# Kernel optimization log

Measured on AMD Instinct MI355X. Metric: run time of the kernel, lower is better.

The kernel has to match this reference:

```python
import jax, jax.numpy as jnp
import numpy as np

B, C, H, W = 32, 256, 56, 56
HIDDEN = 512  # int(channels * hidden_ratio) = int(256 * 2.0)
RANK = 8


def setup_inputs() -> dict:
    key = jax.random.key(0)
    k_x, k1, k2, kA, kB = jax.random.split(key, 5)
    x = jax.random.normal(k_x, (B, C, H, W), dtype=jnp.float32)
    # nn.Linear weights are (out_features, in_features)
    w1 = jax.random.normal(k1, (HIDDEN, C), dtype=jnp.float32) * (1.0 / np.sqrt(C))
    w2 = jax.random.normal(k2, (C, HIDDEN), dtype=jnp.float32) * (1.0 / np.sqrt(HIDDEN))
    wA = jax.random.normal(kA, (H * RANK, C), dtype=jnp.float32) * (1.0 / np.sqrt(C))
    wB = jax.random.normal(kB, (RANK * W, C), dtype=jnp.float32) * (1.0 / np.sqrt(C))
    return {"x": x, "w1": w1, "w2": w2, "wA": wA, "wB": wB}


def reference(x, w1, w2, wA, wB):
    # Global average pool over spatial dims: (B, C)
    y = jnp.mean(x, axis=(2, 3))
    # MLP with exact GELU (dropout = identity at inference)
    h = jax.nn.gelu(y @ w1.T, approximate=False)        # (B, HIDDEN)
    y_prime = jax.nn.gelu(h @ w2.T, approximate=False)  # (B, C)
    # y_rep broadcasts y_prime[b] to every channel, so the per-channel
    # projections are identical across c: compute once per batch.
    A = (y_prime @ wA.T).reshape(B, H, RANK)   # (B, H, r)
    Bm = (y_prime @ wB.T).reshape(B, RANK, W)  # (B, r, W)
    M = jnp.einsum('bik,bkj->bij', A, Bm)      # (B, H, W)
    attn = jax.nn.sigmoid(M)
    # Broadcast identical map across channels -> (B, C, H, W)
    return jnp.broadcast_to(attn[:, None, :, :], (B, C, H, W))
```

## Files before the change

kernel.cpp:

```cpp
#include <hip/hip_runtime.h>
#include <math.h>

#define BB   32
#define CC   256
#define HH   56
#define WW   56
#define HID  512
#define RNK  8
#define HWN  (HH * WW)
#define HW4  (HWN / 4)

__device__ __forceinline__ float gelu_exact(float v) {
    return 0.5f * v * (1.0f + erff(v * 0.70710678118654752f));
}
__device__ __forceinline__ float dot4(float4 a, float4 b) {
    return a.x * b.x + a.y * b.y + a.z * b.z + a.w * b.w;
}

__global__ __launch_bounds__(256) void pool_kernel(const float* __restrict__ x,
                                                   float* __restrict__ y) {
    const int bc  = blockIdx.x;
    const int tid = threadIdx.x;
    const float4* xp = reinterpret_cast<const float4*>(x) + (size_t)bc * HW4;

    float s = 0.0f;
    for (int p = tid; p < HW4; p += 256) {
        float4 v = xp[p];
        s += (v.x + v.y) + (v.z + v.w);
    }
    #pragma unroll
    for (int off = 32; off > 0; off >>= 1) s += __shfl_down(s, off, 64);

    __shared__ float ls[4];
    const int wave = tid >> 6;
    if ((tid & 63) == 0) ls[wave] = s;
    __syncthreads();
    if (tid == 0) {
        float t = (ls[0] + ls[1]) + (ls[2] + ls[3]);
        y[bc] = t * (1.0f / (float)HWN);
    }
}

__global__ __launch_bounds__(1024) void middle_kernel(
        const float* __restrict__ y,  const float* __restrict__ w1,
        const float* __restrict__ w2, const float* __restrict__ wA,
        const float* __restrict__ wB, float* __restrict__ attn) {
    const int b    = blockIdx.x;
    const int tid  = threadIdx.x;
    const int wv   = tid >> 6;
    const int lane = tid & 63;
    const int sub  = lane & 15;
    const int rg   = lane >> 4;

    __shared__ float y_s[CC];
    __shared__ float h_s[HID];
    __shared__ float yp_s[CC];
    __shared__ float ab_s[896];

    if (tid < CC) y_s[tid] = y[b * CC + tid];
    __syncthreads();

    {
        const float4* ys4 = reinterpret_cast<const float4*>(y_s);
        const float4 yv0 = ys4[sub],      yv1 = ys4[sub + 16],
                     yv2 = ys4[sub + 32], yv3 = ys4[sub + 48];
        for (int row = wv * 4 + rg; row < HID; row += 64) {
            const float4* wr = reinterpret_cast<const float4*>(w1 + (size_t)row * CC);
            float d = dot4(wr[sub], yv0)      + dot4(wr[sub + 16], yv1)
                    + dot4(wr[sub + 32], yv2) + dot4(wr[sub + 48], yv3);
            #pragma unroll
            for (int m = 8; m > 0; m >>= 1) d += __shfl_xor(d, m, 64);
            if (sub == 0) h_s[row] = gelu_exact(d);
        }
    }
    __syncthreads();

    {
        const float4* hs4 = reinterpret_cast<const float4*>(h_s);
        float4 hv[8];
        #pragma unroll
        for (int k = 0; k < 8; ++k) hv[k] = hs4[sub + 16 * k];
        for (int row = wv * 4 + rg; row < CC; row += 64) {
            const float4* wr = reinterpret_cast<const float4*>(w2 + (size_t)row * HID);
            float d = 0.0f;
            #pragma unroll
            for (int k = 0; k < 8; ++k) d += dot4(wr[sub + 16 * k], hv[k]);
            #pragma unroll
            for (int m = 8; m > 0; m >>= 1) d += __shfl_xor(d, m, 64);
            if (sub == 0) yp_s[row] = gelu_exact(d);
        }
    }
    __syncthreads();

    {
        const float4* ps4 = reinterpret_cast<const float4*>(yp_s);
        const float4 pv0 = ps4[sub],      pv1 = ps4[sub + 16],
                     pv2 = ps4[sub + 32], pv3 = ps4[sub + 48];
        for (int row = wv * 4 + rg; row < 896; row += 64) {
            const float* W = (row < 448) ? (wA + (size_t)row * CC)
                                         : (wB + (size_t)(row - 448) * CC);
            const float4* wr = reinterpret_cast<const float4*>(W);
            float d = dot4(wr[sub], pv0)      + dot4(wr[sub + 16], pv1)
                    + dot4(wr[sub + 32], pv2) + dot4(wr[sub + 48], pv3);
            #pragma unroll
            for (int m = 8; m > 0; m >>= 1) d += __shfl_xor(d, m, 64);
            if (sub == 0) ab_s[row] = d;
        }
    }
    __syncthreads();

    for (int p = tid; p < HWN; p += 1024) {
        const int i = p / WW;
        const int j = p - i * WW;
        float m = 0.0f;
        #pragma unroll
        for (int r = 0; r < RNK; ++r) m += ab_s[i * RNK + r] * ab_s[448 + r * WW + j];
        attn[(size_t)b * HWN + p] = 1.0f / (1.0f + expf(-m));
    }
}

__global__ __launch_bounds__(256) void bcast_kernel(const float* __restrict__ attn,
                                                    float4* __restrict__ out) {
    const unsigned total  = (unsigned)BB * CC * HW4;
    const unsigned stride = gridDim.x * blockDim.x;
    const float4* ap = reinterpret_cast<const float4*>(attn);
    for (unsigned idx = blockIdx.x * blockDim.x + threadIdx.x; idx < total;
         idx += stride) {
        const unsigned b = idx / (CC * HW4);
        const unsigned p = idx % HW4;
        out[idx] = ap[b * HW4 + p];
    }
}

extern "C" void kernel_launch(void* const* d_in, const int* in_sizes, int n_in,
                              void* d_out, int out_size, void* d_ws, size_t ws_size,
                              hipStream_t stream) {
    const float* x  = (const float*)d_in[0];
    const float* w1 = (const float*)d_in[1];
    const float* w2 = (const float*)d_in[2];
    const float* wA = (const float*)d_in[3];
    const float* wB = (const float*)d_in[4];
    float* out = (float*)d_out;

    float* y    = (float*)d_ws;
    float* attn = y + BB * CC;

    pool_kernel<<<BB * CC, 256, 0, stream>>>(x, y);
    middle_kernel<<<BB, 1024, 0, stream>>>(y, w1, w2, wA, wB, attn);
    bcast_kernel<<<2048, 256, 0, stream>>>(attn, reinterpret_cast<float4*>(out));
}
```

Baseline: 61.72 us.

## Split middle MLP across 8 blocks per batch and fuse attention map into broadcast

The middle kernel now runs 8 blocks per batch. Each block recomputes the two MLP layers with all 1024 threads mapped to rows in fixed passes, then computes only its slice of the wA/wB projection rows. The sigmoid attention map is moved into the broadcast kernel: each block rebuilds the full map in shared memory and writes it to 32 channels, which removes the attn round trip through global memory. In exchange the MLP weights are read 8 times redundantly, and the map is recomputed 8 times per batch.

After: 52.46 us. 15.0% less time.

```diff
diff --git a/kernel.cpp b/kernel.cpp
--- a/kernel.cpp
+++ b/kernel.cpp
@@ -44,69 +44,93 @@
 __global__ __launch_bounds__(1024) void middle_kernel(
         const float* __restrict__ y,  const float* __restrict__ w1,
         const float* __restrict__ w2, const float* __restrict__ wA,
-        const float* __restrict__ wB, float* __restrict__ attn) {
-    const int b    = blockIdx.x;
-    const int tid  = threadIdx.x;
-    const int wv   = tid >> 6;
-    const int lane = tid & 63;
-    const int sub  = lane & 15;
-    const int rg   = lane >> 4;
+        const float* __restrict__ wB, float* __restrict__ ab) {
+    const int b     = blockIdx.x >> 3;
+    const int slice = blockIdx.x & 7;
+    const int tid   = threadIdx.x;
 
     __shared__ float y_s[CC];
     __shared__ float h_s[HID];
     __shared__ float yp_s[CC];
-    __shared__ float ab_s[896];
 
     if (tid < CC) y_s[tid] = y[b * CC + tid];
     __syncthreads();
 
     {
+        const int sub = tid & 7;
+        const int rg  = tid >> 3;
         const float4* ys4 = reinterpret_cast<const float4*>(y_s);
-        const float4 yv0 = ys4[sub],      yv1 = ys4[sub + 16],
-                     yv2 = ys4[sub + 32], yv3 = ys4[sub + 48];
-        for (int row = wv * 4 + rg; row < HID; row += 64) {
+        float4 yv[8];
+        #pragma unroll
+        for (int k = 0; k < 8; ++k) yv[k] = ys4[sub + 8 * k];
+        #pragma unroll
+        for (int pass = 0; pass < 4; ++pass) {
+            const int row = pass * 128 + rg;
             const float4* wr = reinterpret_cast<const float4*>(w1 + (size_t)row * CC);
-            float d = dot4(wr[sub], yv0)      + dot4(wr[sub + 16], yv1)
-                    + dot4(wr[sub + 32], yv2) + dot4(wr[sub + 48], yv3);
+            float d = 0.0f;
             #pragma unroll
-            for (int m = 8; m > 0; m >>= 1) d += __shfl_xor(d, m, 64);
+            for (int k = 0; k < 8; ++k) d += dot4(wr[sub + 8 * k], yv[k]);
+            d += __shfl_xor(d, 1, 64);
+            d += __shfl_xor(d, 2, 64);
+            d += __shfl_xor(d, 4, 64);
             if (sub == 0) h_s[row] = gelu_exact(d);
         }
     }
     __syncthreads();
 
     {
+        const int sub = tid & 15;
+        const int rg  = tid >> 4;
         const float4* hs4 = reinterpret_cast<const float4*>(h_s);
         float4 hv[8];
         #pragma unroll
         for (int k = 0; k < 8; ++k) hv[k] = hs4[sub + 16 * k];
-        for (int row = wv * 4 + rg; row < CC; row += 64) {
+        #pragma unroll
+        for (int pass = 0; pass < 4; ++pass) {
+            const int row = pass * 64 + rg;
             const float4* wr = reinterpret_cast<const float4*>(w2 + (size_t)row * HID);
             float d = 0.0f;
             #pragma unroll
             for (int k = 0; k < 8; ++k) d += dot4(wr[sub + 16 * k], hv[k]);
-            #pragma unroll
-            for (int m = 8; m > 0; m >>= 1) d += __shfl_xor(d, m, 64);
+            d += __shfl_xor(d, 1, 64);
+            d += __shfl_xor(d, 2, 64);
+            d += __shfl_xor(d, 4, 64);
+            d += __shfl_xor(d, 8, 64);
             if (sub == 0) yp_s[row] = gelu_exact(d);
         }
     }
     __syncthreads();
 
     {
-        const float4* ps4 = reinterpret_cast<const float4*>(yp_s);
-        const float4 pv0 = ps4[sub],      pv1 = ps4[sub + 16],
-                     pv2 = ps4[sub + 32], pv3 = ps4[sub + 48];
-        for (int row = wv * 4 + rg; row < 896; row += 64) {
+        const int sub = tid & 7;
+        const int rg  = tid >> 3;
+        if (rg < 112) {
+            const int row = slice * 112 + rg;
             const float* W = (row < 448) ? (wA + (size_t)row * CC)
                                          : (wB + (size_t)(row - 448) * CC);
-            const float4* wr = reinterpret_cast<const float4*>(W);
-            float d = dot4(wr[sub], pv0)      + dot4(wr[sub + 16], pv1)
-                    + dot4(wr[sub + 32], pv2) + dot4(wr[sub + 48], pv3);
+            const float4* wr  = reinterpret_cast<const float4*>(W);
+            const float4* ps4 = reinterpret_cast<const float4*>(yp_s);
+            float d = 0.0f;
             #pragma unroll
-            for (int m = 8; m > 0; m >>= 1) d += __shfl_xor(d, m, 64);
-            if (sub == 0) ab_s[row] = d;
+            for (int k = 0; k < 8; ++k) d += dot4(wr[sub + 8 * k], ps4[sub + 8 * k]);
+            d += __shfl_xor(d, 1, 64);
+            d += __shfl_xor(d, 2, 64);
+            d += __shfl_xor(d, 4, 64);
+            if (sub == 0) ab[(size_t)b * 896 + row] = d;
         }
     }
+}
+
+__global__ __launch_bounds__(1024) void bcast_map_kernel(
+        const float* __restrict__ ab, float4* __restrict__ out) {
+    const int b     = blockIdx.x >> 3;
+    const int slice = blockIdx.x & 7;
+    const int tid   = threadIdx.x;
+
+    __shared__ float ab_s[896];
+    __shared__ float attn_s[HWN];
+
+    if (tid < 896) ab_s[tid] = ab[(size_t)b * 896 + tid];
     __syncthreads();
 
     for (int p = tid; p < HWN; p += 1024) {
@@ -114,21 +138,17 @@
         const int j = p - i * WW;
         float m = 0.0f;
         #pragma unroll
-        for (int r = 0; r < RNK; ++r) m += ab_s[i * RNK + r] * ab_s[448 + r * WW + j];
-        attn[(size_t)b * HWN + p] = 1.0f / (1.0f + expf(-m));
+        for (int r = 0; r < RNK; ++r)
+            m += ab_s[i * RNK + r] * ab_s[448 + r * WW + j];
+        attn_s[p] = 1.0f / (1.0f + expf(-m));
     }
-}
+    __syncthreads();
 
-__global__ __launch_bounds__(256) void bcast_kernel(const float* __restrict__ attn,
-                                                    float4* __restrict__ out) {
-    const unsigned total  = (unsigned)BB * CC * HW4;
-    const unsigned stride = gridDim.x * blockDim.x;
-    const float4* ap = reinterpret_cast<const float4*>(attn);
-    for (unsigned idx = blockIdx.x * blockDim.x + threadIdx.x; idx < total;
-         idx += stride) {
-        const unsigned b = idx / (CC * HW4);
-        const unsigned p = idx % HW4;
-        out[idx] = ap[b * HW4 + p];
+    const float4* a4 = reinterpret_cast<const float4*>(attn_s);
+    float4* base = out + ((size_t)(b * CC + slice * 32)) * HW4;
+    for (int idx = tid; idx < 32 * HW4; idx += 1024) {
+        const int p = idx % HW4;
+        base[idx] = a4[p];
     }
 }
 
@@ -142,10 +162,10 @@
     const float* wB = (const float*)d_in[4];
     float* out = (float*)d_out;
 
-    float* y    = (float*)d_ws;
-    float* attn = y + BB * CC;
+    float* y  = (float*)d_ws;
+    float* ab = y + BB * CC;
 
     pool_kernel<<<BB * CC, 256, 0, stream>>>(x, y);
-    middle_kernel<<<BB, 1024, 0, stream>>>(y, w1, w2, wA, wB, attn);
-    bcast_kernel<<<2048, 256, 0, stream>>>(attn, reinterpret_cast<float4*>(out));
+    middle_kernel<<<BB * 8, 1024, 0, stream>>>(y, w1, w2, wA, wB, ab);
+    bcast_map_kernel<<<BB * 8, 1024, 0, stream>>>(ab, reinterpret_cast<float4*>(out));
 }
```
